# Kernel optimization log

Hardware: AMD Instinct MI355X
Metric: run time of the kernel (lower is better)

The kernel has to match this reference:

```python
import jax, jax.numpy as jnp
import numpy as np

B, N, E, H = 2, 512, 128, 256
IN_DIM = 3 * E + 1


def setup_inputs() -> dict:
    key = jax.random.key(0)
    ks = jax.random.split(key, 9)
    node_embed = jax.random.normal(ks[0], (B, N, E), dtype=jnp.float32)
    problems = jax.random.uniform(ks[1], (B, N, 4), dtype=jnp.float32)
    euclid = jax.random.uniform(ks[2], (B, N, N), dtype=jnp.float32)
    euclid = 0.5 * (euclid + jnp.swapaxes(euclid, 1, 2))  # symmetric, realistic
    s = 0.02
    W1 = s * jax.random.normal(ks[3], (IN_DIM, H), dtype=jnp.float32)
    b1 = jnp.zeros((H,), jnp.float32)
    W2 = s * jax.random.normal(ks[4], (H, H), dtype=jnp.float32)
    b2 = jnp.zeros((H,), jnp.float32)
    W3 = s * jax.random.normal(ks[5], (H, 1), dtype=jnp.float32)
    b3 = jnp.zeros((1,), jnp.float32)
    return {"node_embed": node_embed, "problems": problems,
            "euclid_distance_matrix": euclid,
            "W1": W1, "b1": b1, "W2": W2, "b2": b2, "W3": W3, "b3": b3}


def _forward(node_embed, euclid, W1, b1, W2, b2, W3, b3):
    b, n, e = node_embed.shape
    hi = jnp.broadcast_to(node_embed[:, :, None, :], (b, n, n, e))
    hj = jnp.broadcast_to(node_embed[:, None, :, :], (b, n, n, e))
    habs = jnp.abs(node_embed[:, :, None, :] - node_embed[:, None, :, :])
    x = jnp.concatenate([hi, hj, habs, euclid[..., None]], axis=-1)  # (B,N,N,3E+1)
    h = jax.nn.relu(jnp.einsum('bijf,fh->bijh', x, W1) + b1)
    h = jax.nn.relu(jnp.einsum('bijh,hg->bijg', h, W2) + b2)
    pred = (jnp.einsum('bijh,ho->bijo', h, W3) + b3)[..., 0]  # (B,N,N)
    pred = 0.5 * (pred + jnp.swapaxes(pred, 1, 2))
    pred = pred * (1.0 - jnp.eye(n, dtype=pred.dtype))  # zero diagonal
    return pred


def reference(node_embed, problems, euclid_distance_matrix, W1, b1, W2, b2, W3, b3):
    # euclid_distance_matrix provided, so `problems` fallback path is unused
    return _forward(node_embed, euclid_distance_matrix, W1, b1, W2, b2, W3, b3)
```

## Files before the change

### kernel.cpp

```cpp
#include <hip/hip_runtime.h>
#include <hip/hip_bf16.h>


#define BN 512
#define EE 128
#define HH 256

typedef __attribute__((ext_vector_type(8)))  short short8;
typedef __attribute__((ext_vector_type(16))) float f32x16;
typedef __attribute__((ext_vector_type(4)))  float f32x4;

static __device__ __forceinline__ unsigned short f2bf(float f) {
    __bf16 h = (__bf16)f;
    return __builtin_bit_cast(unsigned short, h);
}
static __device__ __forceinline__ float bf2f(unsigned short s) {
    return (float)__builtin_bit_cast(__bf16, s);
}
static __device__ __forceinline__ f32x16 zero16() {
    f32x16 v;
    #pragma unroll
    for (int i = 0; i < 16; ++i) v[i] = 0.f;
    return v;
}
#define MFMA(a, b, c) __builtin_amdgcn_mfma_f32_32x32x16_bf16((a), (b), (c), 0, 0, 0)

__global__ void pack_all(const float* __restrict__ node, const float* __restrict__ W1,
                         const float* __restrict__ W2, const float* __restrict__ b2,
                         unsigned short* __restrict__ w1c_p, unsigned short* __restrict__ w1b_p,
                         unsigned short* __restrict__ w2_p,  unsigned short* __restrict__ w1d_f,
                         unsigned short* __restrict__ b2_f,  unsigned short* __restrict__ node_p) {
    int idx = blockIdx.x * 256 + threadIdx.x;
    {
        int t = idx & 7, l = (idx >> 3) & 63, kb = (idx >> 9) & 7;
        int j32 = (idx >> 12) & 15, b = (idx >> 16) & 1;
        int j = j32 * 32 + (l & 31), e = kb * 16 + (l >> 5) * 8 + t;
        node_p[idx] = f2bf(node[((size_t)b * BN + j) * EE + e]);
    }
    if (idx < 65536) {
        int t = idx & 7, l = (idx >> 3) & 63, nb = (idx >> 9) & 7, kb = idx >> 12;
        int k = kb * 16 + (l >> 5) * 8 + t, n = nb * 32 + (l & 31);
        w2_p[idx] = f2bf(W2[k * HH + n]);
        if (idx < 32768) {
            w1c_p[idx] = f2bf(W1[(2 * EE + k) * HH + n]);
            w1b_p[idx] = f2bf(W1[(EE + k) * HH + n]);
        }
    }
    if (idx < 4096) {
        int t = idx & 7, l = (idx >> 3) & 63, nb = idx >> 9;
        int n = nb * 32 + (l & 31);
        bool nz = (t == 0 && l < 32);
        w1d_f[idx] = nz ? f2bf(W1[(3 * EE) * HH + n]) : (unsigned short)0;
        b2_f[idx]  = nz ? f2bf(b2[n]) : (unsigned short)0;
    }
}

__global__ void precompute_pa(const float* __restrict__ node, const float* __restrict__ W1,
                              const float* __restrict__ b1, float* __restrict__ PA) {
    int bi = blockIdx.x, h = threadIdx.x;
    const float* nd = node + (size_t)bi * EE;
    float sa = b1[h];
    #pragma unroll 8
    for (int e = 0; e < EE; ++e) sa += nd[e] * W1[e * HH + h];
    PA[bi * HH + h] = sa;
}

__global__ __launch_bounds__(256, 3) void edge_main(
    const float* __restrict__ node, const float* __restrict__ euclid,
    const float* __restrict__ W3, const float* __restrict__ b3,
    const float* __restrict__ PA,
    const unsigned short* __restrict__ w1c_p, const unsigned short* __restrict__ w1b_p,
    const unsigned short* __restrict__ w2_p,  const unsigned short* __restrict__ w1d_f,
    const unsigned short* __restrict__ b2_f,  const unsigned short* __restrict__ node_p,
    float* __restrict__ out)
{
    __shared__ __align__(16) unsigned short lds_buf[64 * 264];
    __shared__ __align__(16) float hi_f[EE];
    __shared__ float pp[256];

    const int jt = blockIdx.x, i = blockIdx.y, b = blockIdx.z;
    const int jbase = jt * 64;
    const int tid = threadIdx.x, wave = tid >> 6, lane = tid & 63;
    const int m0 = lane & 31, kq = (lane >> 5) * 8;

    if (tid < 32)
        ((f32x4*)hi_f)[tid] = ((const f32x4*)(node + ((size_t)b * BN + i) * EE))[tid];
    __syncthreads();

    {
        int row = tid >> 2, q = tid & 3;
        const f32x4* nj = (const f32x4*)(node + ((size_t)b * BN + jbase + row) * EE);
        const f32x4* hv = (const f32x4*)hi_f;
        unsigned short* dst = &lds_buf[row * 136 + q * 32];
        #pragma unroll
        for (int k = 0; k < 4; ++k) {
            f32x4 a0 = nj[q * 8 + k * 2 + 0], h0 = hv[q * 8 + k * 2 + 0];
            f32x4 a1 = nj[q * 8 + k * 2 + 1], h1v = hv[q * 8 + k * 2 + 1];
            short8 pk;
            #pragma unroll
            for (int u = 0; u < 4; ++u) {
                pk[u]     = (short)f2bf(fabsf(a0[u] - h0[u]));
                pk[4 + u] = (short)f2bf(fabsf(a1[u] - h1v[u]));
            }
            *(short8*)(dst + k * 8) = pk;
        }
    }
    __syncthreads();

    f32x16 a00 = zero16(), a01 = zero16(), a10 = zero16(), a11 = zero16();
    {
        const short8* bc = (const short8*)w1c_p;
        const short8* bb = (const short8*)w1b_p;
        const short8* np = (const short8*)node_p + (size_t)(b * 16 + jt * 2) * 8 * 64;
        #pragma unroll
        for (int kb = 0; kb < 8; ++kb) {
            short8 ad0 = *(const short8*)&lds_buf[m0 * 136 + kb * 16 + kq];
            short8 ad1 = *(const short8*)&lds_buf[(m0 + 32) * 136 + kb * 16 + kq];
            short8 ah0 = np[kb * 64 + lane];
            short8 ah1 = np[(8 + kb) * 64 + lane];
            short8 b0 = bc[(kb * 8 + wave * 2 + 0) * 64 + lane];
            short8 b1 = bc[(kb * 8 + wave * 2 + 1) * 64 + lane];
            short8 c0 = bb[(kb * 8 + wave * 2 + 0) * 64 + lane];
            short8 c1 = bb[(kb * 8 + wave * 2 + 1) * 64 + lane];
            a00 = MFMA(ad0, b0, a00); a01 = MFMA(ad0, b1, a01);
            a10 = MFMA(ad1, b0, a10); a11 = MFMA(ad1, b1, a11);
            a00 = MFMA(ah0, c0, a00); a01 = MFMA(ah0, c1, a01);
            a10 = MFMA(ah1, c0, a10); a11 = MFMA(ah1, c1, a11);
        }
        const float* erow = euclid + ((size_t)b * BN + i) * BN + jbase;
        short8 ae0, ae1;
        #pragma unroll
        for (int u = 0; u < 8; ++u) { ae0[u] = 0; ae1[u] = 0; }
        if (lane < 32) {
            ae0[0] = (short)f2bf(erow[m0]);
            ae1[0] = (short)f2bf(erow[32 + m0]);
        }
        short8 d0 = ((const short8*)w1d_f)[(wave * 2 + 0) * 64 + lane];
        short8 d1 = ((const short8*)w1d_f)[(wave * 2 + 1) * 64 + lane];
        a00 = MFMA(ae0, d0, a00); a01 = MFMA(ae0, d1, a01);
        a10 = MFMA(ae1, d0, a10); a11 = MFMA(ae1, d1, a11);
    }
    __syncthreads();

    {
        const float* paRow = PA + ((size_t)b * BN + i) * HH;
        int col0 = wave * 64 + m0;
        float pa0 = paRow[col0], pa1 = paRow[col0 + 32];
        int rbase = 4 * (lane >> 5);
        #pragma unroll
        for (int r = 0; r < 16; ++r) {
            int row = (r & 3) + 8 * (r >> 2) + rbase;
            float v0 = a00[r] + pa0; v0 = v0 > 0.f ? v0 : 0.f;
            float v1 = a01[r] + pa1; v1 = v1 > 0.f ? v1 : 0.f;
            float v2 = a10[r] + pa0; v2 = v2 > 0.f ? v2 : 0.f;
            float v3 = a11[r] + pa1; v3 = v3 > 0.f ? v3 : 0.f;
            lds_buf[row * 264 + col0]             = f2bf(v0);
            lds_buf[row * 264 + col0 + 32]        = f2bf(v1);
            lds_buf[(row + 32) * 264 + col0]      = f2bf(v2);
            lds_buf[(row + 32) * 264 + col0 + 32] = f2bf(v3);
        }
    }
    __syncthreads();

    f32x16 c00 = zero16(), c01 = zero16(), c10 = zero16(), c11 = zero16();
    {
        const short8* bp = (const short8*)w2_p;
        #pragma unroll
        for (int kb = 0; kb < 16; ++kb) {
            short8 ad0 = *(const short8*)&lds_buf[m0 * 264 + kb * 16 + kq];
            short8 ad1 = *(const short8*)&lds_buf[(m0 + 32) * 264 + kb * 16 + kq];
            short8 b0 = bp[(kb * 8 + wave * 2 + 0) * 64 + lane];
            short8 b1 = bp[(kb * 8 + wave * 2 + 1) * 64 + lane];
            c00 = MFMA(ad0, b0, c00); c01 = MFMA(ad0, b1, c01);
            c10 = MFMA(ad1, b0, c10); c11 = MFMA(ad1, b1, c11);
        }
        short8 aone;
        #pragma unroll
        for (int u = 0; u < 8; ++u) aone[u] = 0;
        if (lane < 32) aone[0] = (short)0x3F80;
        short8 e0 = ((const short8*)b2_f)[(wave * 2 + 0) * 64 + lane];
        short8 e1 = ((const short8*)b2_f)[(wave * 2 + 1) * 64 + lane];
        c00 = MFMA(aone, e0, c00); c01 = MFMA(aone, e1, c01);
        c10 = MFMA(aone, e0, c10); c11 = MFMA(aone, e1, c11);
    }
    __syncthreads();

    {
        int col0 = wave * 64 + m0;
        int rbase = 4 * (lane >> 5);
        #pragma unroll
        for (int r = 0; r < 16; ++r) {
            int row = (r & 3) + 8 * (r >> 2) + rbase;
            float v0 = c00[r] > 0.f ? c00[r] : 0.f;
            float v1 = c01[r] > 0.f ? c01[r] : 0.f;
            float v2 = c10[r] > 0.f ? c10[r] : 0.f;
            float v3 = c11[r] > 0.f ? c11[r] : 0.f;
            lds_buf[row * 264 + col0]             = f2bf(v0);
            lds_buf[row * 264 + col0 + 32]        = f2bf(v1);
            lds_buf[(row + 32) * 264 + col0]      = f2bf(v2);
            lds_buf[(row + 32) * 264 + col0 + 32] = f2bf(v3);
        }
    }
    __syncthreads();

    {
        int r = tid & 63, part = tid >> 6, c0 = part * 64;
        float s = 0.f;
        #pragma unroll
        for (int k = 0; k < 8; ++k) {
            short8 h8 = *(const short8*)&lds_buf[r * 264 + c0 + k * 8];
            #pragma unroll
            for (int u = 0; u < 8; ++u)
                s += bf2f((unsigned short)h8[u]) * W3[c0 + k * 8 + u];
        }
        pp[part * 64 + r] = s;
    }
    __syncthreads();
    if (tid < 64) {
        float v = pp[tid] + pp[64 + tid] + pp[128 + tid] + pp[192 + tid] + b3[0];
        out[((size_t)b * BN + i) * BN + jbase + tid] = v;
    }
}

__global__ void symmetrize(float* __restrict__ out) {
    int b = blockIdx.z, ti = blockIdx.y, tj = blockIdx.x;
    if (tj < ti) return;
    int i = ti * 32 + threadIdx.y, j = tj * 32 + threadIdx.x;
    float* p = out + (size_t)b * BN * BN;
    if (i == j) { p[(size_t)i * BN + j] = 0.f; return; }
    if (j < i) return;
    float a = p[(size_t)i * BN + j];
    float c = p[(size_t)j * BN + i];
    float v = 0.5f * (a + c);
    p[(size_t)i * BN + j] = v;
    p[(size_t)j * BN + i] = v;
}

extern "C" void kernel_launch(void* const* d_in, const int* in_sizes, int n_in,
                              void* d_out, int out_size, void* d_ws, size_t ws_size,
                              hipStream_t stream) {
    const float* node   = (const float*)d_in[0];
    const float* euclid = (const float*)d_in[2];
    const float* W1     = (const float*)d_in[3];
    const float* b1     = (const float*)d_in[4];
    const float* W2     = (const float*)d_in[5];
    const float* b2     = (const float*)d_in[6];
    const float* W3     = (const float*)d_in[7];
    const float* b3     = (const float*)d_in[8];
    float* out = (float*)d_out;

    char* ws = (char*)d_ws;
    float*          PA     = (float*)ws;
    unsigned short* w1c_p  = (unsigned short*)(ws + (1u << 20));
    unsigned short* w1b_p  = (unsigned short*)(ws + (1u << 20) + 65536);
    unsigned short* w2_p   = (unsigned short*)(ws + (1u << 20) + 131072);
    unsigned short* w1d_f  = (unsigned short*)(ws + (1u << 20) + 262144);
    unsigned short* b2_f   = (unsigned short*)(ws + (1u << 20) + 270336);
    unsigned short* node_p = (unsigned short*)(ws + (1u << 20) + 278528);

    pack_all<<<512, 256, 0, stream>>>(node, W1, W2, b2, w1c_p, w1b_p, w2_p, w1d_f, b2_f, node_p);
    precompute_pa<<<BN * 2, 256, 0, stream>>>(node, W1, b1, PA);
    edge_main<<<dim3(BN / 64, BN, 2), 256, 0, stream>>>(
        node, euclid, W3, b3, PA, w1c_p, w1b_p, w2_p, w1d_f, b2_f, node_p, out);
    symmetrize<<<dim3(BN / 32, BN / 32, 2), dim3(32, 32), 0, stream>>>(out);
}
```

Baseline: 255.5 us.

## Double edge tile to 128 rows per block and build hj operand in LDS

Each block now handles 128 j-columns instead of 64, so every wave runs four M-tiles per weight fragment and reuses each loaded W1/W2 fragment twice as often. The hj bf16 operand is converted from node into a packed LDS layout inside the kernel, which removes the node_p prepack from pack_all, and the euclid row is staged in LDS. The cost is double the LDS use and more accumulators, with launch bounds lowered from 3 to 2 blocks per SM, so occupancy falls.

```diff
diff --git a/kernel.cpp b/kernel.cpp
--- a/kernel.cpp
+++ b/kernel.cpp
@@ -25,19 +25,13 @@
 }
 #define MFMA(a, b, c) __builtin_amdgcn_mfma_f32_32x32x16_bf16((a), (b), (c), 0, 0, 0)
 
-__global__ void pack_all(const float* __restrict__ node, const float* __restrict__ W1,
-                         const float* __restrict__ W2, const float* __restrict__ b2,
+__global__ void pack_all(const float* __restrict__ W1, const float* __restrict__ W2,
+                         const float* __restrict__ b2,
                          unsigned short* __restrict__ w1c_p, unsigned short* __restrict__ w1b_p,
                          unsigned short* __restrict__ w2_p,  unsigned short* __restrict__ w1d_f,
-                         unsigned short* __restrict__ b2_f,  unsigned short* __restrict__ node_p) {
+                         unsigned short* __restrict__ b2_f) {
     int idx = blockIdx.x * 256 + threadIdx.x;
     {
-        int t = idx & 7, l = (idx >> 3) & 63, kb = (idx >> 9) & 7;
-        int j32 = (idx >> 12) & 15, b = (idx >> 16) & 1;
-        int j = j32 * 32 + (l & 31), e = kb * 16 + (l >> 5) * 8 + t;
-        node_p[idx] = f2bf(node[((size_t)b * BN + j) * EE + e]);
-    }
-    if (idx < 65536) {
         int t = idx & 7, l = (idx >> 3) & 63, nb = (idx >> 9) & 7, kb = idx >> 12;
         int k = kb * 16 + (l >> 5) * 8 + t, n = nb * 32 + (l & 31);
         w2_p[idx] = f2bf(W2[k * HH + n]);
@@ -65,80 +59,91 @@
     PA[bi * HH + h] = sa;
 }
 
-__global__ __launch_bounds__(256, 3) void edge_main(
+__global__ __launch_bounds__(256, 2) void edge_main(
     const float* __restrict__ node, const float* __restrict__ euclid,
     const float* __restrict__ W3, const float* __restrict__ b3,
     const float* __restrict__ PA,
     const unsigned short* __restrict__ w1c_p, const unsigned short* __restrict__ w1b_p,
     const unsigned short* __restrict__ w2_p,  const unsigned short* __restrict__ w1d_f,
-    const unsigned short* __restrict__ b2_f,  const unsigned short* __restrict__ node_p,
+    const unsigned short* __restrict__ b2_f,
     float* __restrict__ out)
 {
-    __shared__ __align__(16) unsigned short lds_buf[64 * 264];
+    __shared__ __align__(16) unsigned short lds_buf[128 * 264];
     __shared__ __align__(16) float hi_f[EE];
+    __shared__ float lds_e[128];
     __shared__ float pp[256];
 
     const int jt = blockIdx.x, i = blockIdx.y, b = blockIdx.z;
-    const int jbase = jt * 64;
+    const int jbase = jt * 128;
     const int tid = threadIdx.x, wave = tid >> 6, lane = tid & 63;
-    const int m0 = lane & 31, kq = (lane >> 5) * 8;
+    const int m0 = lane & 31, q = lane >> 5, kq = q * 8;
+    unsigned short* hjb = lds_buf + 128 * 136;
 
     if (tid < 32)
         ((f32x4*)hi_f)[tid] = ((const f32x4*)(node + ((size_t)b * BN + i) * EE))[tid];
-    __syncthreads();
-
-    {
-        int row = tid >> 2, q = tid & 3;
+    if (tid < 128)
+        lds_e[tid] = euclid[((size_t)b * BN + i) * BN + jbase + tid];
+    __syncthreads();
+
+    {
+        int row = tid >> 1, half = tid & 1;
         const f32x4* nj = (const f32x4*)(node + ((size_t)b * BN + jbase + row) * EE);
         const f32x4* hv = (const f32x4*)hi_f;
-        unsigned short* dst = &lds_buf[row * 136 + q * 32];
-        #pragma unroll
-        for (int k = 0; k < 4; ++k) {
-            f32x4 a0 = nj[q * 8 + k * 2 + 0], h0 = hv[q * 8 + k * 2 + 0];
-            f32x4 a1 = nj[q * 8 + k * 2 + 1], h1v = hv[q * 8 + k * 2 + 1];
-            short8 pk;
+        int mt = row >> 5, r31 = row & 31;
+        #pragma unroll
+        for (int g = 0; g < 8; ++g) {
+            int c0 = half * 64 + g * 8;
+            f32x4 a0 = nj[c0 / 4], a1 = nj[c0 / 4 + 1];
+            f32x4 h0 = hv[c0 / 4], h1v = hv[c0 / 4 + 1];
+            short8 pd, ph;
             #pragma unroll
             for (int u = 0; u < 4; ++u) {
-                pk[u]     = (short)f2bf(fabsf(a0[u] - h0[u]));
-                pk[4 + u] = (short)f2bf(fabsf(a1[u] - h1v[u]));
-            }
-            *(short8*)(dst + k * 8) = pk;
-        }
-    }
-    __syncthreads();
-
-    f32x16 a00 = zero16(), a01 = zero16(), a10 = zero16(), a11 = zero16();
-    {
-        const short8* bc = (const short8*)w1c_p;
-        const short8* bb = (const short8*)w1b_p;
-        const short8* np = (const short8*)node_p + (size_t)(b * 16 + jt * 2) * 8 * 64;
+                pd[u]     = (short)f2bf(fabsf(a0[u] - h0[u]));
+                pd[4 + u] = (short)f2bf(fabsf(a1[u] - h1v[u]));
+                ph[u]     = (short)f2bf(a0[u]);
+                ph[4 + u] = (short)f2bf(a1[u]);
+            }
+            *(short8*)&lds_buf[row * 136 + c0] = pd;
+            int kb = c0 >> 4, hk = (c0 >> 3) & 1;
+            *(short8*)&hjb[((mt * 8 + kb) * 64 + r31 + 32 * hk) * 8] = ph;
+        }
+    }
+    __syncthreads();
+
+    f32x16 acc[4][2];
+    #pragma unroll
+    for (int mt = 0; mt < 4; ++mt) { acc[mt][0] = zero16(); acc[mt][1] = zero16(); }
+    {
+        const short8* bc  = (const short8*)w1c_p;
+        const short8* bb  = (const short8*)w1b_p;
+        const short8* hjf = (const short8*)hjb;
         #pragma unroll
         for (int kb = 0; kb < 8; ++kb) {
-            short8 ad0 = *(const short8*)&lds_buf[m0 * 136 + kb * 16 + kq];
-            short8 ad1 = *(const short8*)&lds_buf[(m0 + 32) * 136 + kb * 16 + kq];
-            short8 ah0 = np[kb * 64 + lane];
-            short8 ah1 = np[(8 + kb) * 64 + lane];
             short8 b0 = bc[(kb * 8 + wave * 2 + 0) * 64 + lane];
             short8 b1 = bc[(kb * 8 + wave * 2 + 1) * 64 + lane];
             short8 c0 = bb[(kb * 8 + wave * 2 + 0) * 64 + lane];
             short8 c1 = bb[(kb * 8 + wave * 2 + 1) * 64 + lane];
-            a00 = MFMA(ad0, b0, a00); a01 = MFMA(ad0, b1, a01);
-            a10 = MFMA(ad1, b0, a10); a11 = MFMA(ad1, b1, a11);
-            a00 = MFMA(ah0, c0, a00); a01 = MFMA(ah0, c1, a01);
-            a10 = MFMA(ah1, c0, a10); a11 = MFMA(ah1, c1, a11);
-        }
-        const float* erow = euclid + ((size_t)b * BN + i) * BN + jbase;
-        short8 ae0, ae1;
-        #pragma unroll
-        for (int u = 0; u < 8; ++u) { ae0[u] = 0; ae1[u] = 0; }
-        if (lane < 32) {
-            ae0[0] = (short)f2bf(erow[m0]);
-            ae1[0] = (short)f2bf(erow[32 + m0]);
+            #pragma unroll
+            for (int mt = 0; mt < 4; ++mt) {
+                short8 ad = *(const short8*)&lds_buf[(mt * 32 + m0) * 136 + kb * 16 + kq];
+                short8 ah = hjf[(mt * 8 + kb) * 64 + lane];
+                acc[mt][0] = MFMA(ad, b0, acc[mt][0]);
+                acc[mt][1] = MFMA(ad, b1, acc[mt][1]);
+                acc[mt][0] = MFMA(ah, c0, acc[mt][0]);
+                acc[mt][1] = MFMA(ah, c1, acc[mt][1]);
+            }
         }
         short8 d0 = ((const short8*)w1d_f)[(wave * 2 + 0) * 64 + lane];
         short8 d1 = ((const short8*)w1d_f)[(wave * 2 + 1) * 64 + lane];
-        a00 = MFMA(ae0, d0, a00); a01 = MFMA(ae0, d1, a01);
-        a10 = MFMA(ae1, d0, a10); a11 = MFMA(ae1, d1, a11);
+        #pragma unroll
+        for (int mt = 0; mt < 4; ++mt) {
+            short8 ae;
+            #pragma unroll
+            for (int u = 0; u < 8; ++u) ae[u] = 0;
+            if (lane < 32) ae[0] = (short)f2bf(lds_e[mt * 32 + m0]);
+            acc[mt][0] = MFMA(ae, d0, acc[mt][0]);
+            acc[mt][1] = MFMA(ae, d1, acc[mt][1]);
+        }
     }
     __syncthreads();
 
@@ -146,33 +151,36 @@
         const float* paRow = PA + ((size_t)b * BN + i) * HH;
         int col0 = wave * 64 + m0;
         float pa0 = paRow[col0], pa1 = paRow[col0 + 32];
-        int rbase = 4 * (lane >> 5);
-        #pragma unroll
-        for (int r = 0; r < 16; ++r) {
-            int row = (r & 3) + 8 * (r >> 2) + rbase;
-            float v0 = a00[r] + pa0; v0 = v0 > 0.f ? v0 : 0.f;
-            float v1 = a01[r] + pa1; v1 = v1 > 0.f ? v1 : 0.f;
-            float v2 = a10[r] + pa0; v2 = v2 > 0.f ? v2 : 0.f;
-            float v3 = a11[r] + pa1; v3 = v3 > 0.f ? v3 : 0.f;
-            lds_buf[row * 264 + col0]             = f2bf(v0);
-            lds_buf[row * 264 + col0 + 32]        = f2bf(v1);
-            lds_buf[(row + 32) * 264 + col0]      = f2bf(v2);
-            lds_buf[(row + 32) * 264 + col0 + 32] = f2bf(v3);
-        }
-    }
-    __syncthreads();
-
-    f32x16 c00 = zero16(), c01 = zero16(), c10 = zero16(), c11 = zero16();
+        int rq = 4 * q;
+        #pragma unroll
+        for (int mt = 0; mt < 4; ++mt) {
+            #pragma unroll
+            for (int r = 0; r < 16; ++r) {
+                int row = mt * 32 + (r & 3) + 8 * (r >> 2) + rq;
+                float v0 = acc[mt][0][r] + pa0; v0 = v0 > 0.f ? v0 : 0.f;
+                float v1 = acc[mt][1][r] + pa1; v1 = v1 > 0.f ? v1 : 0.f;
+                lds_buf[row * 264 + col0]      = f2bf(v0);
+                lds_buf[row * 264 + col0 + 32] = f2bf(v1);
+            }
+        }
+    }
+    __syncthreads();
+
+    f32x16 c2[4][2];
+    #pragma unroll
+    for (int mt = 0; mt < 4; ++mt) { c2[mt][0] = zero16(); c2[mt][1] = zero16(); }
     {
         const short8* bp = (const short8*)w2_p;
         #pragma unroll
         for (int kb = 0; kb < 16; ++kb) {
-            short8 ad0 = *(const short8*)&lds_buf[m0 * 264 + kb * 16 + kq];
-            short8 ad1 = *(const short8*)&lds_buf[(m0 + 32) * 264 + kb * 16 + kq];
             short8 b0 = bp[(kb * 8 + wave * 2 + 0) * 64 + lane];
             short8 b1 = bp[(kb * 8 + wave * 2 + 1) * 64 + lane];
-            c00 = MFMA(ad0, b0, c00); c01 = MFMA(ad0, b1, c01);
-            c10 = MFMA(ad1, b0, c10); c11 = MFMA(ad1, b1, c11);
+            #pragma unroll
+            for (int mt = 0; mt < 4; ++mt) {
+                short8 a = *(const short8*)&lds_buf[(mt * 32 + m0) * 264 + kb * 16 + kq];
+                c2[mt][0] = MFMA(a, b0, c2[mt][0]);
+                c2[mt][1] = MFMA(a, b1, c2[mt][1]);
+            }
         }
         short8 aone;
         #pragma unroll
@@ -180,44 +188,46 @@
         if (lane < 32) aone[0] = (short)0x3F80;
         short8 e0 = ((const short8*)b2_f)[(wave * 2 + 0) * 64 + lane];
         short8 e1 = ((const short8*)b2_f)[(wave * 2 + 1) * 64 + lane];
-        c00 = MFMA(aone, e0, c00); c01 = MFMA(aone, e1, c01);
-        c10 = MFMA(aone, e0, c10); c11 = MFMA(aone, e1, c11);
+        #pragma unroll
+        for (int mt = 0; mt < 4; ++mt) {
+            c2[mt][0] = MFMA(aone, e0, c2[mt][0]);
+            c2[mt][1] = MFMA(aone, e1, c2[mt][1]);
+        }
     }
     __syncthreads();
 
     {
         int col0 = wave * 64 + m0;
-        int rbase = 4 * (lane >> 5);
-        #pragma unroll
-        for (int r = 0; r < 16; ++r) {
-            int row = (r & 3) + 8 * (r >> 2) + rbase;
-            float v0 = c00[r] > 0.f ? c00[r] : 0.f;
-            float v1 = c01[r] > 0.f ? c01[r] : 0.f;
-            float v2 = c10[r] > 0.f ? c10[r] : 0.f;
-            float v3 = c11[r] > 0.f ? c11[r] : 0.f;
-            lds_buf[row * 264 + col0]             = f2bf(v0);
-            lds_buf[row * 264 + col0 + 32]        = f2bf(v1);
-            lds_buf[(row + 32) * 264 + col0]      = f2bf(v2);
-            lds_buf[(row + 32) * 264 + col0 + 32] = f2bf(v3);
-        }
-    }
-    __syncthreads();
-
-    {
-        int r = tid & 63, part = tid >> 6, c0 = part * 64;
+        int rq = 4 * q;
+        #pragma unroll
+        for (int mt = 0; mt < 4; ++mt) {
+            #pragma unroll
+            for (int r = 0; r < 16; ++r) {
+                int row = mt * 32 + (r & 3) + 8 * (r >> 2) + rq;
+                float v0 = c2[mt][0][r] > 0.f ? c2[mt][0][r] : 0.f;
+                float v1 = c2[mt][1][r] > 0.f ? c2[mt][1][r] : 0.f;
+                lds_buf[row * 264 + col0]      = f2bf(v0);
+                lds_buf[row * 264 + col0 + 32] = f2bf(v1);
+            }
+        }
+    }
+    __syncthreads();
+
+    {
+        int row = tid >> 1, halfc = (tid & 1) * 128;
         float s = 0.f;
         #pragma unroll
-        for (int k = 0; k < 8; ++k) {
-            short8 h8 = *(const short8*)&lds_buf[r * 264 + c0 + k * 8];
+        for (int k = 0; k < 16; ++k) {
+            short8 h8 = *(const short8*)&lds_buf[row * 264 + halfc + k * 8];
             #pragma unroll
             for (int u = 0; u < 8; ++u)
-                s += bf2f((unsigned short)h8[u]) * W3[c0 + k * 8 + u];
-        }
-        pp[part * 64 + r] = s;
-    }
-    __syncthreads();
-    if (tid < 64) {
-        float v = pp[tid] + pp[64 + tid] + pp[128 + tid] + pp[192 + tid] + b3[0];
+                s += bf2f((unsigned short)h8[u]) * W3[halfc + k * 8 + u];
+        }
+        pp[tid] = s;
+    }
+    __syncthreads();
+    if (tid < 128) {
+        float v = pp[tid * 2] + pp[tid * 2 + 1] + b3[0];
         out[((size_t)b * BN + i) * BN + jbase + tid] = v;
     }
 }
@@ -250,17 +260,16 @@
     float* out = (float*)d_out;
 
     char* ws = (char*)d_ws;
-    float*          PA     = (float*)ws;
-    unsigned short* w1c_p  = (unsigned short*)(ws + (1u << 20));
-    unsigned short* w1b_p  = (unsigned short*)(ws + (1u << 20) + 65536);
-    unsigned short* w2_p   = (unsigned short*)(ws + (1u << 20) + 131072);
-    unsigned short* w1d_f  = (unsigned short*)(ws + (1u << 20) + 262144);
-    unsigned short* b2_f   = (unsigned short*)(ws + (1u << 20) + 270336);
-    unsigned short* node_p = (unsigned short*)(ws + (1u << 20) + 278528);
-
-    pack_all<<<512, 256, 0, stream>>>(node, W1, W2, b2, w1c_p, w1b_p, w2_p, w1d_f, b2_f, node_p);
+    float*          PA    = (float*)ws;
+    unsigned short* w1c_p = (unsigned short*)(ws + (1u << 20));
+    unsigned short* w1b_p = (unsigned short*)(ws + (1u << 20) + 65536);
+    unsigned short* w2_p  = (unsigned short*)(ws + (1u << 20) + 131072);
+    unsigned short* w1d_f = (unsigned short*)(ws + (1u << 20) + 262144);
+    unsigned short* b2_f  = (unsigned short*)(ws + (1u << 20) + 270336);
+
+    pack_all<<<256, 256, 0, stream>>>(W1, W2, b2, w1c_p, w1b_p, w2_p, w1d_f, b2_f);
     precompute_pa<<<BN * 2, 256, 0, stream>>>(node, W1, b1, PA);
-    edge_main<<<dim3(BN / 64, BN, 2), 256, 0, stream>>>(
-        node, euclid, W3, b3, PA, w1c_p, w1b_p, w2_p, w1d_f, b2_f, node_p, out);
+    edge_main<<<dim3(BN / 128, BN, 2), 256, 0, stream>>>(
+        node, euclid, W3, b3, PA, w1c_p, w1b_p, w2_p, w1d_f, b2_f, out);
     symmetrize<<<dim3(BN / 32, BN / 32, 2), dim3(32, 32), 0, stream>>>(out);
 }
```

After: 243.7 us. -4.6%, faster.
